# Kernel optimization log

Hardware: AMD Instinct MI355X
Metric: run time of the kernel (lower is better)

The kernel has to match this reference:

```python
import jax, jax.numpy as jnp
import numpy as np

B, T, E, A = 16, 512, 256, 8

def setup_inputs() -> dict:
    key = jax.random.key(0)
    k1, k2, k3, k4, k5 = jax.random.split(key, 5)
    sent_feat = jax.random.normal(k1, (B, T, E), dtype=jnp.float32)
    mask = jax.random.randint(k2, (B, T), 0, 2, dtype=jnp.int32)
    atr_scores = jax.random.uniform(k3, (B, A), dtype=jnp.float32)
    W = jax.random.normal(k4, (E, A * E), dtype=jnp.float32) * 0.02  # nn.Linear weight (out, in)
    b = jax.random.normal(k5, (E,), dtype=jnp.float32) * 0.02
    return {"sent_feat": sent_feat, "mask": mask, "atr_scores": atr_scores, "W": W, "b": b}

def reference(sent_feat, mask, atr_scores, W, b):
    Bb, Tt, Ee = sent_feat.shape
    Aa = atr_scores.shape[1]
    sqrt_dim = jnp.float32(np.sqrt(Ee))
    # scale per-attribute copies of the sentence features: (B,A,T,E)
    sf = sent_feat[:, None, :, :] * atr_scores[:, :, None, None]
    sf = sf.reshape(Bb * Aa, Tt, Ee)
    # scaled dot-product scores (B*A, T, T)
    score = jnp.einsum('bte,bse->bts', sf, sf) / sqrt_dim
    # outer-product mask: bmm(mask[:,:,1], mask[:,1,:]) -> bool, repeat over A
    mf = mask.astype(jnp.float32)
    m2 = (mf[:, :, None] * mf[:, None, :]) != 0.0  # (B,T,T)
    m2 = jnp.broadcast_to(m2[:, None, :, :], (Bb, Aa, Tt, Tt)).reshape(Bb * Aa, Tt, Tt)
    # masked_fill_ fills score with 0.0 where mask == 0 (NOT -inf, faithful to source)
    score = jnp.where(m2, score, jnp.float32(0.0))
    # softmax(score - global_max) over last axis
    attn = jax.nn.softmax(score - jnp.max(score), axis=-1)
    attn_out = jnp.einsum('bts,bse->bte', attn, sf)  # (B*A, T, E)
    attn_out = attn_out.reshape(Bb, Tt, Aa * Ee)
    output = attn_out @ W.T + b  # (B, T, E)
    return (output, attn)
```

## Files before the change

kernel.cpp:

```cpp
#include <hip/hip_runtime.h>
#include <hip/hip_bf16.h>


#define Bt 16
#define Tt 512
#define Et 256
#define At 8

typedef __attribute__((ext_vector_type(8))) short short8;
typedef __attribute__((ext_vector_type(4))) float floatx4;

static __device__ __forceinline__ unsigned short f2bf(float x) {
    union { float f; unsigned u; } v; v.f = x;
    unsigned r = v.u + 0x7fffu + ((v.u >> 16) & 1u);
    return (unsigned short)(r >> 16);
}

static __device__ __forceinline__ floatx4 mfma16(short8 a, short8 b, floatx4 c) {
    return __builtin_amdgcn_mfma_f32_16x16x32_bf16(a, b, c, 0, 0, 0);
}

static __device__ __forceinline__ void barrier_lds() {
    __builtin_amdgcn_sched_barrier(0);
    asm volatile("s_waitcnt lgkmcnt(0)" ::: "memory");
    __builtin_amdgcn_s_barrier();
    __builtin_amdgcn_sched_barrier(0);
}

__global__ __launch_bounds__(256) void k_prep_sent(const float* __restrict__ sent,
                                                   unsigned short* __restrict__ sentG,
                                                   unsigned short* __restrict__ sentFB) {
    int bb = blockIdx.z;
    int s0 = blockIdx.x * 32;
    int e0 = blockIdx.y * 32;
    __shared__ float tile[32][33];
    int c  = threadIdx.x & 31;
    int r4 = threadIdx.x >> 5;
    for (int i = 0; i < 4; ++i) {
        int r = r4 + 8 * i;
        tile[r][c] = sent[(bb * Tt + s0 + r) * Et + e0 + c];
    }
    __syncthreads();
    int wv = threadIdx.x >> 6, lane = threadIdx.x & 63, quad = lane >> 4, l16 = lane & 15;
    union { short8 s; unsigned short e[8]; } u;
    if (wv < 2) {
#pragma unroll
        for (int j = 0; j < 8; ++j) u.e[j] = f2bf(tile[wv * 16 + l16][quad * 8 + j]);
        *(short8*)(sentG + (((size_t)(bb * 32 + (s0 >> 4) + wv)) * 8 + (e0 >> 5)) * 512
                   + lane * 8) = u.s;
    } else {
        int h = wv - 2;
#pragma unroll
        for (int j = 0; j < 8; ++j) u.e[j] = f2bf(tile[quad * 8 + j][h * 16 + l16]);
        *(short8*)(sentFB + (((size_t)(bb * 16 + (e0 >> 4) + h)) * 16 + (s0 >> 5)) * 512
                   + lane * 8) = u.s;
    }
}

__global__ __launch_bounds__(256) void k_prep_w(const float* __restrict__ W,
                                                unsigned short* __restrict__ Wp) {
    int nt = blockIdx.x;
    int pc = blockIdx.y;
    int wave = threadIdx.x >> 6, lane = threadIdx.x & 63, quad = lane >> 4, l16 = lane & 15;
    const int KK = At * Et;
    for (int p = pc * 2; p < pc * 2 + 2; ++p) {
        int kc = wave + 4 * p;
        const float* src = W + (size_t)(nt * 16 + l16) * KK + kc * 32 + quad * 8;
        union { short8 s; unsigned short e[8]; } u;
#pragma unroll
        for (int j = 0; j < 8; ++j) u.e[j] = f2bf(src[j]);
        *(short8*)(Wp + (((size_t)nt * 64 + kc) << 9) + lane * 8) = u.s;
    }
}

__global__ __launch_bounds__(256) void k_attnpv(const unsigned short* __restrict__ sentG,
                                                const unsigned short* __restrict__ sentFB,
                                                const int* __restrict__ mask,
                                                const float* __restrict__ atr,
                                                float* __restrict__ attnf,
                                                unsigned short* __restrict__ Xws) {
    int hw = blockIdx.x;
    int logical = (hw & 7) * 128 + (hw >> 3);
    int z  = logical >> 9;
    int bb = (logical >> 5) & 15;
    int t0 = (logical & 31) * 16;
    int a0 = z * 4;
    __shared__ float S[16][516];
    __shared__ float msk[512];
    __shared__ float mrowv[16];
    unsigned short* Pb = (unsigned short*)&S[0][0];
    unsigned short* Xb = Pb + 8192;

    int tid = threadIdx.x;
    for (int i = tid; i < 512; i += 256) msk[i] = (mask[bb * Tt + i] != 0) ? 1.0f : 0.0f;
    if (tid < 16) mrowv[tid] = (mask[bb * Tt + t0 + tid] != 0) ? 1.0f : 0.0f;
    barrier_lds();

    int wv = tid >> 6, lane = tid & 63, quad = lane >> 4, l16 = lane & 15;

    const unsigned short* Gbase = sentG + ((size_t)(bb * 32 + (t0 >> 4)) * 8) * 512 + lane * 8;
    short8 af[8];
#pragma unroll
    for (int kk = 0; kk < 8; ++kk) af[kk] = *(const short8*)(Gbase + kk * 512);

#pragma unroll
    for (int i = 0; i < 8; ++i) {
        int nt = wv * 8 + i;
        const unsigned short* Bb = sentG + ((size_t)(bb * 32 + nt) * 8) * 512 + lane * 8;
        floatx4 c = {0.f, 0.f, 0.f, 0.f};
#pragma unroll
        for (int kk = 0; kk < 8; ++kk)
            c = mfma16(af[kk], *(const short8*)(Bb + kk * 512), c);
#pragma unroll
        for (int r = 0; r < 4; ++r) {
            int cidx = nt * 16 + l16;
            S[quad * 4 + r][cidx] = c[r] * msk[cidx] * mrowv[quad * 4 + r];
        }
    }
    barrier_lds();

    int row = tid >> 4, cl = tid & 15;
    float w[32];
    float wmax = -1e30f;
#pragma unroll
    for (int i4 = 0; i4 < 8; ++i4) {
        float4 v = *(const float4*)&S[row][i4 * 64 + cl * 4];
        w[i4 * 4 + 0] = v.x; w[i4 * 4 + 1] = v.y; w[i4 * 4 + 2] = v.z; w[i4 * 4 + 3] = v.w;
        wmax = fmaxf(wmax, fmaxf(fmaxf(v.x, v.y), fmaxf(v.z, v.w)));
    }
#pragma unroll
    for (int off = 8; off >= 1; off >>= 1) wmax = fmaxf(wmax, __shfl_xor(wmax, off, 64));
    barrier_lds();

    for (int a = a0; a < a0 + 4; ++a) {
        float av = atr[bb * At + a];
        float coef = av * av * (1.0f / 16.0f);
        float mx = coef * wmax;
        float p[32];
        float sum = 0.f;
#pragma unroll
        for (int j = 0; j < 32; ++j) {
            float e = __expf(fmaf(coef, w[j], -mx));
            p[j] = e;
            sum += e;
        }
#pragma unroll
        for (int off = 8; off >= 1; off >>= 1) sum += __shfl_xor(sum, off, 64);
        float inv = 1.0f / sum;
#pragma unroll
        for (int j = 0; j < 32; ++j) p[j] *= inv;

        float* orow = attnf + ((size_t)(bb * At + a) * Tt + (t0 + row)) * Tt;
#pragma unroll
        for (int i4 = 0; i4 < 8; ++i4) {
            float4 v;
            v.x = p[i4 * 4 + 0]; v.y = p[i4 * 4 + 1];
            v.z = p[i4 * 4 + 2]; v.w = p[i4 * 4 + 3];
            *(float4*)(orow + i4 * 64 + cl * 4) = v;
        }

#pragma unroll
        for (int i4 = 0; i4 < 8; ++i4) {
            unsigned b0 = __float_as_uint(p[i4 * 4 + 0]) + 0x8000u;
            unsigned b1 = __float_as_uint(p[i4 * 4 + 1]) + 0x8000u;
            unsigned b2 = __float_as_uint(p[i4 * 4 + 2]) + 0x8000u;
            unsigned b3 = __float_as_uint(p[i4 * 4 + 3]) + 0x8000u;
            uint2 pk;
            pk.x = __builtin_amdgcn_perm(b1, b0, 0x07060302u);
            pk.y = __builtin_amdgcn_perm(b3, b2, 0x07060302u);
            int h = i4 * 8 + (cl >> 1);
            *(uint2*)(Pb + row * 512 + ((h ^ (row & 7)) << 3) + (cl & 1) * 4) = pk;
        }
        barrier_lds();

        floatx4 pacc[4];
#pragma unroll
        for (int i = 0; i < 4; ++i) pacc[i] = (floatx4){0.f, 0.f, 0.f, 0.f};
        for (int kc = 0; kc < 16; ++kc) {
            short8 afr = *(const short8*)(Pb + l16 * 512 +
                (((kc * 4 + quad) ^ (l16 & 7)) << 3));
#pragma unroll
            for (int i = 0; i < 4; ++i) {
                short8 bfr = *(const short8*)(sentFB +
                    (((size_t)(bb * 16 + wv * 4 + i) * 16 + kc) << 9) + lane * 8);
                pacc[i] = mfma16(afr, bfr, pacc[i]);
            }
        }

#pragma unroll
        for (int i = 0; i < 4; ++i) {
            int e = (wv * 4 + i) * 16 + l16;
#pragma unroll
            for (int r = 0; r < 4; ++r) {
                int tl = quad * 4 + r;
                Xb[(tl >> 3) * 2048 + (tl & 7) * 256 + e] = f2bf(av * pacc[i][r]);
            }
        }
        barrier_lds();

        {
            size_t xbase = ((size_t)bb * Tt + a * 64 + (t0 >> 3)) * 2048;
            int g = tid >> 7, off = (tid & 127) * 16;
            short8 v0 = *(const short8*)(Xb + g * 2048 + off);
            short8 v1 = *(const short8*)(Xb + g * 2048 + off + 8);
            *(short8*)(Xws + xbase + g * 2048 + off) = v0;
            *(short8*)(Xws + xbase + g * 2048 + off + 8) = v1;
        }
    }
}

__global__ __launch_bounds__(512) void k_out(const unsigned short* __restrict__ Xws,
                                             const unsigned short* __restrict__ Wp,
                                             const float* __restrict__ bias,
                                             float* __restrict__ out) {
    int bb = blockIdx.y;
    int tp0 = blockIdx.x * 16;
    int tid = threadIdx.x;
    int wv = tid >> 6, lane = tid & 63, quad = lane >> 4, l16 = lane & 15;

    __shared__ unsigned short Xb[16 * 2048];

    int rhat = tid >> 5;
    int hb   = tid & 31;
    const unsigned short* src = Xws + ((size_t)bb * Tt + tp0 + rhat) * 2048;
#pragma unroll
    for (int p = 0; p < 8; ++p) {
        int h = hb + 32 * p;
        short8 v = *(const short8*)(src + h * 8);
        *(short8*)(Xb + rhat * 2048 + ((h ^ (rhat & 7)) << 3)) = v;
    }
    __syncthreads();

    floatx4 oacc[2];
#pragma unroll
    for (int i = 0; i < 2; ++i) oacc[i] = (floatx4){0.f, 0.f, 0.f, 0.f};

    const int KK = At * Et;
#pragma unroll 4
    for (int k0 = 0; k0 < KK; k0 += 32) {
        short8 afr = *(const short8*)(Xb + l16 * 2048 +
            ((((k0 >> 3) + quad) ^ (l16 & 7)) << 3));
#pragma unroll
        for (int i = 0; i < 2; ++i) {
            short8 bf = *(const short8*)(Wp +
                (((size_t)(wv * 2 + i) * 64 + (k0 >> 5)) << 9) + lane * 8);
            oacc[i] = mfma16(afr, bf, oacc[i]);
        }
    }
#pragma unroll
    for (int i = 0; i < 2; ++i) {
        int n = (wv * 2 + i) * 16 + l16;
        float bv = bias[n];
#pragma unroll
        for (int r = 0; r < 4; ++r) {
            int tp = tp0 + quad * 4 + r;
            out[((size_t)bb * Tt + tp) * Et + n] = oacc[i][r] + bv;
        }
    }
}

extern "C" void kernel_launch(void* const* d_in, const int* in_sizes, int n_in,
                              void* d_out, int out_size, void* d_ws, size_t ws_size,
                              hipStream_t stream) {
    const float* sent = (const float*)d_in[0];
    const int*   mask = (const int*)d_in[1];
    const float* atr  = (const float*)d_in[2];
    const float* W    = (const float*)d_in[3];
    const float* bias = (const float*)d_in[4];

    float* out0  = (float*)d_out;
    float* attnf = out0 + (size_t)Bt * Tt * Et;

    char* ws = (char*)d_ws;
    unsigned short* sentG  = (unsigned short*)(ws);
    unsigned short* sentFB = (unsigned short*)(ws + 4194304);
    unsigned short* Wp     = (unsigned short*)(ws + 8388608);
    unsigned short* Xws    = (unsigned short*)(ws + 9437184);

    hipLaunchKernelGGL(k_prep_sent, dim3(Tt / 32, Et / 32, Bt), dim3(256), 0, stream,
                       sent, sentG, sentFB);
    hipLaunchKernelGGL(k_prep_w, dim3(16, 8), dim3(256), 0, stream, W, Wp);
    hipLaunchKernelGGL(k_attnpv, dim3(1024), dim3(256), 0, stream,
                       sentG, sentFB, mask, atr, attnf, Xws);
    hipLaunchKernelGGL(k_out, dim3(Tt / 16, Bt), dim3(512), 0, stream,
                       Xws, Wp, bias, out0);
}
```

Baseline: 220.0 us.

## Process attribute pairs per PV pass and widen k_out waves to four N-tiles

```diff
diff --git a/kernel.cpp b/kernel.cpp
--- a/kernel.cpp
+++ b/kernel.cpp
@@ -89,7 +89,7 @@
     __shared__ float msk[512];
     __shared__ float mrowv[16];
     unsigned short* Pb = (unsigned short*)&S[0][0];
-    unsigned short* Xb = Pb + 8192;
+    unsigned short* Xb = (unsigned short*)&S[0][0];
 
     int tid = threadIdx.x;
     for (int i = tid; i < 512; i += 256) msk[i] = (mask[bb * Tt + i] != 0) ? 1.0f : 0.0f;
@@ -132,84 +132,105 @@
     for (int off = 8; off >= 1; off >>= 1) wmax = fmaxf(wmax, __shfl_xor(wmax, off, 64));
     barrier_lds();
 
-    for (int a = a0; a < a0 + 4; ++a) {
-        float av = atr[bb * At + a];
-        float coef = av * av * (1.0f / 16.0f);
-        float mx = coef * wmax;
-        float p[32];
-        float sum = 0.f;
-#pragma unroll
-        for (int j = 0; j < 32; ++j) {
-            float e = __expf(fmaf(coef, w[j], -mx));
-            p[j] = e;
-            sum += e;
-        }
-#pragma unroll
-        for (int off = 8; off >= 1; off >>= 1) sum += __shfl_xor(sum, off, 64);
-        float inv = 1.0f / sum;
-#pragma unroll
-        for (int j = 0; j < 32; ++j) p[j] *= inv;
-
-        float* orow = attnf + ((size_t)(bb * At + a) * Tt + (t0 + row)) * Tt;
-#pragma unroll
-        for (int i4 = 0; i4 < 8; ++i4) {
-            float4 v;
-            v.x = p[i4 * 4 + 0]; v.y = p[i4 * 4 + 1];
-            v.z = p[i4 * 4 + 2]; v.w = p[i4 * 4 + 3];
-            *(float4*)(orow + i4 * 64 + cl * 4) = v;
-        }
-
-#pragma unroll
-        for (int i4 = 0; i4 < 8; ++i4) {
-            unsigned b0 = __float_as_uint(p[i4 * 4 + 0]) + 0x8000u;
-            unsigned b1 = __float_as_uint(p[i4 * 4 + 1]) + 0x8000u;
-            unsigned b2 = __float_as_uint(p[i4 * 4 + 2]) + 0x8000u;
-            unsigned b3 = __float_as_uint(p[i4 * 4 + 3]) + 0x8000u;
-            uint2 pk;
-            pk.x = __builtin_amdgcn_perm(b1, b0, 0x07060302u);
-            pk.y = __builtin_amdgcn_perm(b3, b2, 0x07060302u);
-            int h = i4 * 8 + (cl >> 1);
-            *(uint2*)(Pb + row * 512 + ((h ^ (row & 7)) << 3) + (cl & 1) * 4) = pk;
+    for (int ph = 0; ph < 2; ++ph) {
+        int ap = a0 + ph * 2;
+
+#pragma unroll
+        for (int ai = 0; ai < 2; ++ai) {
+            int a = ap + ai;
+            float av = atr[bb * At + a];
+            float coef = av * av * (1.0f / 16.0f);
+            float mx = coef * wmax;
+            float p[32];
+            float sum = 0.f;
+#pragma unroll
+            for (int j = 0; j < 32; ++j) {
+                float e = __expf(fmaf(coef, w[j], -mx));
+                p[j] = e;
+                sum += e;
+            }
+#pragma unroll
+            for (int off = 8; off >= 1; off >>= 1) sum += __shfl_xor(sum, off, 64);
+            float inv = 1.0f / sum;
+#pragma unroll
+            for (int j = 0; j < 32; ++j) p[j] *= inv;
+
+            float* orow = attnf + ((size_t)(bb * At + a) * Tt + (t0 + row)) * Tt;
+#pragma unroll
+            for (int i4 = 0; i4 < 8; ++i4) {
+                float4 v;
+                v.x = p[i4 * 4 + 0]; v.y = p[i4 * 4 + 1];
+                v.z = p[i4 * 4 + 2]; v.w = p[i4 * 4 + 3];
+                *(float4*)(orow + i4 * 64 + cl * 4) = v;
+            }
+
+#pragma unroll
+            for (int i4 = 0; i4 < 8; ++i4) {
+                unsigned b0 = __float_as_uint(p[i4 * 4 + 0]) + 0x8000u;
+                unsigned b1 = __float_as_uint(p[i4 * 4 + 1]) + 0x8000u;
+                unsigned b2 = __float_as_uint(p[i4 * 4 + 2]) + 0x8000u;
+                unsigned b3 = __float_as_uint(p[i4 * 4 + 3]) + 0x8000u;
+                uint2 pk;
+                pk.x = __builtin_amdgcn_perm(b1, b0, 0x07060302u);
+                pk.y = __builtin_amdgcn_perm(b3, b2, 0x07060302u);
+                int h = i4 * 8 + (cl >> 1);
+                *(uint2*)(Pb + ai * 8192 + row * 512 + ((h ^ (row & 7)) << 3)
+                          + (cl & 1) * 4) = pk;
+            }
         }
         barrier_lds();
 
-        floatx4 pacc[4];
-#pragma unroll
-        for (int i = 0; i < 4; ++i) pacc[i] = (floatx4){0.f, 0.f, 0.f, 0.f};
+        floatx4 pc0[4], pc1[4];
+#pragma unroll
+        for (int i = 0; i < 4; ++i) {
+            pc0[i] = (floatx4){0.f, 0.f, 0.f, 0.f};
+            pc1[i] = (floatx4){0.f, 0.f, 0.f, 0.f};
+        }
         for (int kc = 0; kc < 16; ++kc) {
-            short8 afr = *(const short8*)(Pb + l16 * 512 +
-                (((kc * 4 + quad) ^ (l16 & 7)) << 3));
+            int poff = l16 * 512 + (((kc * 4 + quad) ^ (l16 & 7)) << 3);
+            short8 af0 = *(const short8*)(Pb + poff);
+            short8 af1 = *(const short8*)(Pb + 8192 + poff);
 #pragma unroll
             for (int i = 0; i < 4; ++i) {
                 short8 bfr = *(const short8*)(sentFB +
                     (((size_t)(bb * 16 + wv * 4 + i) * 16 + kc) << 9) + lane * 8);
-                pacc[i] = mfma16(afr, bfr, pacc[i]);
-            }
-        }
-
-#pragma unroll
-        for (int i = 0; i < 4; ++i) {
-            int e = (wv * 4 + i) * 16 + l16;
-#pragma unroll
-            for (int r = 0; r < 4; ++r) {
-                int tl = quad * 4 + r;
-                Xb[(tl >> 3) * 2048 + (tl & 7) * 256 + e] = f2bf(av * pacc[i][r]);
+                pc0[i] = mfma16(af0, bfr, pc0[i]);
+                pc1[i] = mfma16(af1, bfr, pc1[i]);
             }
         }
         barrier_lds();
 
-        {
+#pragma unroll
+        for (int ai = 0; ai < 2; ++ai) {
+            float av = atr[bb * At + ap + ai];
+#pragma unroll
+            for (int i = 0; i < 4; ++i) {
+                int e = (wv * 4 + i) * 16 + l16;
+#pragma unroll
+                for (int r = 0; r < 4; ++r) {
+                    int tl = quad * 4 + r;
+                    float x = av * (ai ? pc1[i][r] : pc0[i][r]);
+                    Xb[ai * 4096 + (tl >> 3) * 2048 + (tl & 7) * 256 + e] = f2bf(x);
+                }
+            }
+        }
+        barrier_lds();
+
+#pragma unroll
+        for (int ai = 0; ai < 2; ++ai) {
+            int a = ap + ai;
             size_t xbase = ((size_t)bb * Tt + a * 64 + (t0 >> 3)) * 2048;
             int g = tid >> 7, off = (tid & 127) * 16;
-            short8 v0 = *(const short8*)(Xb + g * 2048 + off);
-            short8 v1 = *(const short8*)(Xb + g * 2048 + off + 8);
+            short8 v0 = *(const short8*)(Xb + ai * 4096 + g * 2048 + off);
+            short8 v1 = *(const short8*)(Xb + ai * 4096 + g * 2048 + off + 8);
             *(short8*)(Xws + xbase + g * 2048 + off) = v0;
             *(short8*)(Xws + xbase + g * 2048 + off + 8) = v1;
         }
-    }
-}
-
-__global__ __launch_bounds__(512) void k_out(const unsigned short* __restrict__ Xws,
+        barrier_lds();
+    }
+}
+
+__global__ __launch_bounds__(256) void k_out(const unsigned short* __restrict__ Xws,
                                              const unsigned short* __restrict__ Wp,
                                              const float* __restrict__ bias,
                                              float* __restrict__ out) {
@@ -220,20 +241,20 @@
 
     __shared__ unsigned short Xb[16 * 2048];
 
-    int rhat = tid >> 5;
-    int hb   = tid & 31;
+    int rhat = tid >> 4;
+    int hb   = tid & 15;
     const unsigned short* src = Xws + ((size_t)bb * Tt + tp0 + rhat) * 2048;
 #pragma unroll
-    for (int p = 0; p < 8; ++p) {
-        int h = hb + 32 * p;
+    for (int p = 0; p < 16; ++p) {
+        int h = hb + 16 * p;
         short8 v = *(const short8*)(src + h * 8);
         *(short8*)(Xb + rhat * 2048 + ((h ^ (rhat & 7)) << 3)) = v;
     }
     __syncthreads();
 
-    floatx4 oacc[2];
-#pragma unroll
-    for (int i = 0; i < 2; ++i) oacc[i] = (floatx4){0.f, 0.f, 0.f, 0.f};
+    floatx4 oacc[4];
+#pragma unroll
+    for (int i = 0; i < 4; ++i) oacc[i] = (floatx4){0.f, 0.f, 0.f, 0.f};
 
     const int KK = At * Et;
 #pragma unroll 4
@@ -241,15 +262,15 @@
         short8 afr = *(const short8*)(Xb + l16 * 2048 +
             ((((k0 >> 3) + quad) ^ (l16 & 7)) << 3));
 #pragma unroll
-        for (int i = 0; i < 2; ++i) {
+        for (int i = 0; i < 4; ++i) {
             short8 bf = *(const short8*)(Wp +
-                (((size_t)(wv * 2 + i) * 64 + (k0 >> 5)) << 9) + lane * 8);
+                (((size_t)(wv * 4 + i) * 64 + (k0 >> 5)) << 9) + lane * 8);
             oacc[i] = mfma16(afr, bf, oacc[i]);
         }
     }
 #pragma unroll
-    for (int i = 0; i < 2; ++i) {
-        int n = (wv * 2 + i) * 16 + l16;
+    for (int i = 0; i < 4; ++i) {
+        int n = (wv * 4 + i) * 16 + l16;
         float bv = bias[n];
 #pragma unroll
         for (int r = 0; r < 4; ++r) {
@@ -282,6 +303,6 @@
     hipLaunchKernelGGL(k_prep_w, dim3(16, 8), dim3(256), 0, stream, W, Wp);
     hipLaunchKernelGGL(k_attnpv, dim3(1024), dim3(256), 0, stream,
                        sentG, sentFB, mask, atr, attnf, Xws);
-    hipLaunchKernelGGL(k_out, dim3(Tt / 16, Bt), dim3(512), 0, stream,
+    hipLaunchKernelGGL(k_out, dim3(Tt / 16, Bt), dim3(256), 0, stream,
                        Xws, Wp, bias, out0);
 }
```

Measured after the change: 277.9 us. 26.3% more time.

## Store attention output in MFMA fragment layout and read it directly in output GEMM

Applied to the files above, without the earlier changes.

```diff
diff --git a/kernel.cpp b/kernel.cpp
--- a/kernel.cpp
+++ b/kernel.cpp
@@ -78,18 +78,18 @@
                                                 const int* __restrict__ mask,
                                                 const float* __restrict__ atr,
                                                 float* __restrict__ attnf,
-                                                unsigned short* __restrict__ Xws) {
+                                                unsigned short* __restrict__ XwsF) {
     int hw = blockIdx.x;
     int logical = (hw & 7) * 128 + (hw >> 3);
-    int z  = logical >> 9;
-    int bb = (logical >> 5) & 15;
+    int bb = logical >> 6;
+    int z  = (logical >> 5) & 1;
     int t0 = (logical & 31) * 16;
     int a0 = z * 4;
     __shared__ float S[16][516];
     __shared__ float msk[512];
     __shared__ float mrowv[16];
-    unsigned short* Pb = (unsigned short*)&S[0][0];
-    unsigned short* Xb = Pb + 8192;
+    unsigned short* Pb  = (unsigned short*)&S[0][0];
+    unsigned short* Xb2 = Pb + 8192;
 
     int tid = threadIdx.x;
     for (int i = tid; i < 512; i += 256) msk[i] = (mask[bb * Tt + i] != 0) ? 1.0f : 0.0f;
@@ -131,6 +131,8 @@
 #pragma unroll
     for (int off = 8; off >= 1; off >>= 1) wmax = fmaxf(wmax, __shfl_xor(wmax, off, 64));
     barrier_lds();
+
+    int L = (t0 >> 3) & 15;
 
     for (int a = a0; a < a0 + 4; ++a) {
         float av = atr[bb * At + a];
@@ -189,71 +191,65 @@
 
 #pragma unroll
         for (int i = 0; i < 4; ++i) {
-            int e = (wv * 4 + i) * 16 + l16;
+            int W16 = wv * 4 + i;
+            int kcb = W16 >> 1;
+            int qp  = (W16 & 1) * 2 + (l16 >> 3);
+            int jp  = l16 & 7;
 #pragma unroll
             for (int r = 0; r < 4; ++r) {
                 int tl = quad * 4 + r;
-                Xb[(tl >> 3) * 2048 + (tl & 7) * 256 + e] = f2bf(av * pacc[i][r]);
+                Xb2[(((tl & 7) * 8 + kcb) << 6) + qp * 16 + ((tl >> 3) << 3) + jp]
+                    = f2bf(av * pacc[i][r]);
             }
         }
         barrier_lds();
 
         {
-            size_t xbase = ((size_t)bb * Tt + a * 64 + (t0 >> 3)) * 2048;
-            int g = tid >> 7, off = (tid & 127) * 16;
-            short8 v0 = *(const short8*)(Xb + g * 2048 + off);
-            short8 v1 = *(const short8*)(Xb + g * 2048 + off + 8);
-            *(short8*)(Xws + xbase + g * 2048 + off) = v0;
-            *(short8*)(Xws + xbase + g * 2048 + off + 8) = v1;
-        }
-    }
-}
-
-__global__ __launch_bounds__(512) void k_out(const unsigned short* __restrict__ Xws,
+            int kc = tid >> 2, qp = tid & 3;
+            int TPT = (a << 2) + (t0 >> 7);
+            size_t base = (((size_t)(bb * 32 + TPT)) * 64 + kc) * 512;
+            short8 v0 = *(const short8*)(Xb2 + (kc << 6) + qp * 16);
+            short8 v1 = *(const short8*)(Xb2 + (kc << 6) + qp * 16 + 8);
+            *(short8*)(XwsF + base + (qp * 16 + L) * 8)     = v0;
+            *(short8*)(XwsF + base + (qp * 16 + L + 1) * 8) = v1;
+        }
+    }
+}
+
+__global__ __launch_bounds__(256) void k_out(const unsigned short* __restrict__ XwsF,
                                              const unsigned short* __restrict__ Wp,
                                              const float* __restrict__ bias,
                                              float* __restrict__ out) {
-    int bb = blockIdx.y;
-    int tp0 = blockIdx.x * 16;
+    int hw = blockIdx.x;
+    int logical = (hw & 7) * 128 + (hw >> 3);
+    int bb  = logical >> 6;
+    int TPT = (logical >> 1) & 31;
+    int nh  = logical & 1;
     int tid = threadIdx.x;
     int wv = tid >> 6, lane = tid & 63, quad = lane >> 4, l16 = lane & 15;
 
-    __shared__ unsigned short Xb[16 * 2048];
-
-    int rhat = tid >> 5;
-    int hb   = tid & 31;
-    const unsigned short* src = Xws + ((size_t)bb * Tt + tp0 + rhat) * 2048;
-#pragma unroll
-    for (int p = 0; p < 8; ++p) {
-        int h = hb + 32 * p;
-        short8 v = *(const short8*)(src + h * 8);
-        *(short8*)(Xb + rhat * 2048 + ((h ^ (rhat & 7)) << 3)) = v;
-    }
-    __syncthreads();
-
+    const unsigned short* Abase = XwsF + ((size_t)(bb * 32 + TPT)) * 64 * 512 + lane * 8;
     floatx4 oacc[2];
-#pragma unroll
-    for (int i = 0; i < 2; ++i) oacc[i] = (floatx4){0.f, 0.f, 0.f, 0.f};
-
-    const int KK = At * Et;
+    oacc[0] = (floatx4){0.f, 0.f, 0.f, 0.f};
+    oacc[1] = (floatx4){0.f, 0.f, 0.f, 0.f};
+    int nt0 = nh * 8 + wv * 2;
 #pragma unroll 4
-    for (int k0 = 0; k0 < KK; k0 += 32) {
-        short8 afr = *(const short8*)(Xb + l16 * 2048 +
-            ((((k0 >> 3) + quad) ^ (l16 & 7)) << 3));
+    for (int kc = 0; kc < 64; ++kc) {
+        short8 afr = *(const short8*)(Abase + kc * 512);
 #pragma unroll
         for (int i = 0; i < 2; ++i) {
             short8 bf = *(const short8*)(Wp +
-                (((size_t)(wv * 2 + i) * 64 + (k0 >> 5)) << 9) + lane * 8);
+                (((size_t)(nt0 + i) * 64 + kc) << 9) + lane * 8);
             oacc[i] = mfma16(afr, bf, oacc[i]);
         }
     }
 #pragma unroll
     for (int i = 0; i < 2; ++i) {
-        int n = (wv * 2 + i) * 16 + l16;
+        int n = (nt0 + i) * 16 + l16;
         float bv = bias[n];
 #pragma unroll
         for (int r = 0; r < 4; ++r) {
-            int tp = tp0 + quad * 4 + r;
+            int tp = TPT * 16 + quad * 4 + r;
             out[((size_t)bb * Tt + tp) * Et + n] = oacc[i][r] + bv;
         }
     }
@@ -275,13 +271,13 @@
     unsigned short* sentG  = (unsigned short*)(ws);
     unsigned short* sentFB = (unsigned short*)(ws + 4194304);
     unsigned short* Wp     = (unsigned short*)(ws + 8388608);
-    unsigned short* Xws    = (unsigned short*)(ws + 9437184);
+    unsigned short* XwsF   = (unsigned short*)(ws + 9437184);
 
     hipLaunchKernelGGL(k_prep_sent, dim3(Tt / 32, Et / 32, Bt), dim3(256), 0, stream,
                        sent, sentG, sentFB);
     hipLaunchKernelGGL(k_prep_w, dim3(16, 8), dim3(256), 0, stream, W, Wp);
     hipLaunchKernelGGL(k_attnpv, dim3(1024), dim3(256), 0, stream,
-                       sentG, sentFB, mask, atr, attnf, Xws);
-    hipLaunchKernelGGL(k_out, dim3(Tt / 16, Bt), dim3(512), 0, stream,
-                       Xws, Wp, bias, out0);
-}
+                       sentG, sentFB, mask, atr, attnf, XwsF);
+    hipLaunchKernelGGL(k_out, dim3(1024), dim3(256), 0, stream,
+                       XwsF, Wp, bias, out0);
+}
```

Result: slower. 232.6 us (+5.7%).
